# Performance work log

Measured on AMD Instinct MI355X. Metric: run time of the kernel, lower is better.

The kernel has to match this reference:

```python
import jax, jax.numpy as jnp
import numpy as np

B, S, D, KC = 32, 4096, 64, 256  # batch*heads, seq_len, head_dim, compressed dim


def setup_inputs() -> dict:
    key = jax.random.key(0)
    ks = jax.random.split(key, 7)
    return {
        "Q": jax.random.normal(ks[0], (B, S, D), dtype=jnp.float32),
        "K": jax.random.normal(ks[1], (B, S, D), dtype=jnp.float32),
        "V": jax.random.normal(ks[2], (B, S, D), dtype=jnp.float32),
        "E_w": jax.random.normal(ks[3], (KC, S), dtype=jnp.float32) * (1.0 / np.sqrt(S)),
        "E_b": jax.random.normal(ks[4], (KC,), dtype=jnp.float32) * 0.01,
        "F_w": jax.random.normal(ks[5], (KC, S), dtype=jnp.float32) * (1.0 / np.sqrt(S)),
        "F_b": jax.random.normal(ks[6], (KC,), dtype=jnp.float32) * 0.01,
    }


def reference(Q, K, V, E_w, E_b, F_w, F_b):
    # K: [B,S,D] -> transpose -> [B,D,S]; E proj over seq axis -> [B,D,KC]
    Ke = jnp.einsum("bsd,ks->bdk", K, E_w) + E_b  # [B, D, KC]
    # scores: Q @ E(K) -> [B, S, KC], scaled by sqrt(head_dim)
    scale = jnp.sqrt(jnp.asarray(D, dtype=Q.dtype))
    P = jnp.einsum("bsd,bdk->bsk", Q, Ke) / scale
    # causal mask: torch.triu(ones(S, KC)) keeps (i, j) where j >= i
    i = jnp.arange(S)[:, None]
    j = jnp.arange(KC)[None, :]
    keep = j >= i  # [S, KC]
    P = jnp.where(keep[None, :, :], P, jnp.asarray(-1e10, dtype=P.dtype))
    P = jax.nn.softmax(P, axis=-1)  # dropout p=0.0 -> identity
    # V: [B,S,D] -> [B,D,S]; F proj -> [B,D,KC]; transpose -> [B,KC,D]
    Vf = jnp.einsum("bsd,ks->bkd", V, F_w) + F_b[None, :, None]  # [B, KC, D]
    out = jnp.einsum("bsk,bkd->bsd", P, Vf)  # [B, S, D]
    return out
```

## Files before the change

kernel.cpp:

```cpp
#include <hip/hip_runtime.h>
#include <hip/hip_bf16.h>
#include <math.h>

#define NB  32
#define NS  4096
#define ND  64
#define NKC 256
#define ASTR 72
#define PSTR 260
#define PBSTR 264

typedef __attribute__((ext_vector_type(8))) short short8;
typedef __attribute__((ext_vector_type(4))) short sv4;
typedef __attribute__((ext_vector_type(4))) float f32x4;

__device__ __forceinline__ short f2bf(float f) {
    union { float f; unsigned u; } v; v.f = f;
    return (short)((v.u + 0x7FFFu + ((v.u >> 16) & 1u)) >> 16);
}
__device__ __forceinline__ float bf2f(short s) {
    union { unsigned u; float f; } v;
    v.u = ((unsigned)(unsigned short)s) << 16; return v.f;
}

__global__ __launch_bounds__(256) void proj_gemm(
    const float* __restrict__ Ew, const float* __restrict__ Fw,
    const float* __restrict__ K,  const float* __restrict__ V,
    float* __restrict__ KeT, float* __restrict__ Vf)
{
    const int b     = blockIdx.x;
    const int chunk = blockIdx.y;
    const int z     = blockIdx.z;
    const int mt = z >> 1, mm = z & 1;
    const float* __restrict__ A  = mm ? Fw : Ew;
    const float* __restrict__ Bg = mm ? V  : K;
    float* __restrict__ Cout     = mm ? Vf : KeT;

    const int t = threadIdx.x, wave = t >> 6, lane = t & 63;
    const int lm = lane & 15, g = lane >> 4;
    __shared__ short As[64 * ASTR];
    __shared__ short Bs[64 * ASTR];
    const int k0 = mt * 64;
    const size_t bBase = (size_t)b * NS * ND;

    f32x4 acc[4];
#pragma unroll
    for (int i = 0; i < 4; ++i) acc[i] = (f32x4){0.f, 0.f, 0.f, 0.f};

    for (int s0 = chunk * 1024; s0 < chunk * 1024 + 1024; s0 += 64) {
#pragma unroll
        for (int i = 0; i < 4; ++i) {
            int row = i * 16 + (t >> 4), q = t & 15;
            float4 v = *(const float4*)&A[(size_t)(k0 + row) * NS + s0 + q * 4];
            sv4 sv; sv.x = f2bf(v.x); sv.y = f2bf(v.y); sv.z = f2bf(v.z); sv.w = f2bf(v.w);
            *(sv4*)&As[row * ASTR + q * 4] = sv;
        }
        {
            int dB = t & 31, sB = t >> 5;
            float2 v[8];
#pragma unroll
            for (int i = 0; i < 8; ++i)
                v[i] = *(const float2*)&Bg[bBase + (size_t)(s0 + sB * 8 + i) * ND + dB * 2];
            short8 w0, w1;
#pragma unroll
            for (int i = 0; i < 8; ++i) { w0[i] = f2bf(v[i].x); w1[i] = f2bf(v[i].y); }
            *(short8*)&Bs[(dB * 2 + 0) * ASTR + sB * 8] = w0;
            *(short8*)&Bs[(dB * 2 + 1) * ASTR + sB * 8] = w1;
        }
        __syncthreads();
#pragma unroll
        for (int ks = 0; ks < 64; ks += 32) {
            short8 a = *(const short8*)&As[(wave * 16 + lm) * ASTR + ks + g * 8];
#pragma unroll
            for (int nt = 0; nt < 4; ++nt) {
                short8 bb = *(const short8*)&Bs[(nt * 16 + lm) * ASTR + ks + g * 8];
                acc[nt] = __builtin_amdgcn_mfma_f32_16x16x32_bf16(a, bb, acc[nt], 0, 0, 0);
            }
        }
        __syncthreads();
    }
#pragma unroll
    for (int r = 0; r < 4; ++r) {
        int kc = k0 + wave * 16 + g * 4 + r;
#pragma unroll
        for (int nt = 0; nt < 4; ++nt)
            atomicAdd(&Cout[((size_t)b * NKC + kc) * ND + nt * 16 + lm], acc[nt][r]);
    }
}

__global__ __launch_bounds__(256) void convert_bias(
    const float* __restrict__ KeT, const float* __restrict__ Vf,
    const float* __restrict__ Eb,  const float* __restrict__ Fb,
    short* __restrict__ KeTb, short* __restrict__ VfTb)
{
    const int b = blockIdx.y, t = threadIdx.x;
    const int k = blockIdx.x * 32 + (t >> 3), dq = t & 7;
    const size_t off = ((size_t)b * NKC + k) * ND + dq * 8;

    float4 a0 = *(const float4*)&KeT[off], a1 = *(const float4*)&KeT[off + 4];
    float eb = Eb[k];
    short8 w;
    w[0] = f2bf(a0.x + eb); w[1] = f2bf(a0.y + eb); w[2] = f2bf(a0.z + eb); w[3] = f2bf(a0.w + eb);
    w[4] = f2bf(a1.x + eb); w[5] = f2bf(a1.y + eb); w[6] = f2bf(a1.z + eb); w[7] = f2bf(a1.w + eb);
    *(short8*)&KeTb[off] = w;

    float4 v0 = *(const float4*)&Vf[off], v1 = *(const float4*)&Vf[off + 4];
    float fb = Fb[k];
    float vv[8] = {v0.x, v0.y, v0.z, v0.w, v1.x, v1.y, v1.z, v1.w};
#pragma unroll
    for (int j = 0; j < 8; ++j)
        VfTb[((size_t)b * ND + dq * 8 + j) * NKC + k] = f2bf(vv[j] + fb);
}

__global__ __launch_bounds__(256) void attn_fused(
    const float* __restrict__ Q, const short* __restrict__ KeTb,
    const short* __restrict__ VfTb, float* __restrict__ out)
{
    const int x = blockIdx.x, b = blockIdx.y, t = threadIdx.x;

    if (x >= 8) {
        const int ch = x - 8;
        __shared__ float part[4][65];
        __shared__ float mv[64];
        const int d = t >> 2, seg = t & 3;
        const short* vp = &VfTb[((size_t)b * ND + d) * NKC + seg * 64];
        float s = 0.f;
#pragma unroll
        for (int i = 0; i < 8; ++i) {
            short8 h = *(const short8*)&vp[i * 8];
#pragma unroll
            for (int j = 0; j < 8; ++j) s += bf2f(h[j]);
        }
        part[seg][d] = s;
        __syncthreads();
        if (t < 64)
            mv[t] = (part[0][t] + part[1][t] + part[2][t] + part[3][t]) * (1.f / 256.f);
        __syncthreads();
#pragma unroll
        for (int i = 0; i < 15; ++i) {
            int idx = i * 256 + t, row = idx >> 4, q = idx & 15;
            *(float4*)&out[((size_t)b * NS + 256 + ch * 240 + row) * ND + q * 4] =
                *(const float4*)&mv[q * 4];
        }
        return;
    }

    const int s0 = x * 32;
    const int wave = t >> 6, lane = t & 63, lm = lane & 15, g = lane >> 4;
    __shared__ short Qs[32 * ASTR];
    __shared__ float Ps[32 * PSTR];
    __shared__ short PsB[32 * PBSTR];

    {
        int row = t >> 3, dq = t & 7;
        size_t off = ((size_t)b * NS + s0 + row) * ND + dq * 8;
        float4 q0 = *(const float4*)&Q[off], q1 = *(const float4*)&Q[off + 4];
        short8 w;
        w[0] = f2bf(q0.x); w[1] = f2bf(q0.y); w[2] = f2bf(q0.z); w[3] = f2bf(q0.w);
        w[4] = f2bf(q1.x); w[5] = f2bf(q1.y); w[6] = f2bf(q1.z); w[7] = f2bf(q1.w);
        *(short8*)&Qs[row * ASTR + dq * 8] = w;
    }
    __syncthreads();

    const int rt = wave & 1, kh = wave >> 1;
#pragma unroll
    for (int kk = 0; kk < 8; ++kk) {
        int kt = kh * 8 + kk;
        f32x4 acc = (f32x4){0.f, 0.f, 0.f, 0.f};
#pragma unroll
        for (int ks = 0; ks < 64; ks += 32) {
            short8 a  = *(const short8*)&Qs[(rt * 16 + lm) * ASTR + ks + g * 8];
            short8 bb = *(const short8*)&KeTb[((size_t)b * NKC + kt * 16 + lm) * ND + ks + g * 8];
            acc = __builtin_amdgcn_mfma_f32_16x16x32_bf16(a, bb, acc, 0, 0, 0);
        }
        int col = kt * 16 + lm;
#pragma unroll
        for (int r = 0; r < 4; ++r) {
            int rowg = s0 + rt * 16 + g * 4 + r;
            Ps[(rt * 16 + g * 4 + r) * PSTR + col] =
                (col >= rowg) ? acc[r] * 0.125f : -1e30f;
        }
    }
    __syncthreads();

    for (int rr = wave * 8; rr < wave * 8 + 8; ++rr) {
        float v0 = Ps[rr * PSTR + lane],       v1 = Ps[rr * PSTR + lane + 64];
        float v2 = Ps[rr * PSTR + lane + 128], v3 = Ps[rr * PSTR + lane + 192];
        float m = fmaxf(fmaxf(v0, v1), fmaxf(v2, v3));
        for (int off = 32; off; off >>= 1) m = fmaxf(m, __shfl_xor(m, off, 64));
        float e0 = __expf(v0 - m), e1 = __expf(v1 - m);
        float e2 = __expf(v2 - m), e3 = __expf(v3 - m);
        float s = e0 + e1 + e2 + e3;
        for (int off = 32; off; off >>= 1) s += __shfl_xor(s, off, 64);
        float inv = 1.f / s;
        PsB[rr * PBSTR + lane]       = f2bf(e0 * inv);
        PsB[rr * PBSTR + lane + 64]  = f2bf(e1 * inv);
        PsB[rr * PBSTR + lane + 128] = f2bf(e2 * inv);
        PsB[rr * PBSTR + lane + 192] = f2bf(e3 * inv);
    }
    __syncthreads();

    const int dt = wave;
    f32x4 oa[2];
    oa[0] = (f32x4){0.f, 0.f, 0.f, 0.f};
    oa[1] = (f32x4){0.f, 0.f, 0.f, 0.f};
    for (int ks = x; ks < 8; ++ks) {
        short8 bb = *(const short8*)&VfTb[((size_t)b * ND + dt * 16 + lm) * NKC + ks * 32 + g * 8];
#pragma unroll
        for (int r2 = 0; r2 < 2; ++r2) {
            short8 a = *(const short8*)&PsB[(r2 * 16 + lm) * PBSTR + ks * 32 + g * 8];
            oa[r2] = __builtin_amdgcn_mfma_f32_16x16x32_bf16(a, bb, oa[r2], 0, 0, 0);
        }
    }
#pragma unroll
    for (int r2 = 0; r2 < 2; ++r2)
#pragma unroll
        for (int r = 0; r < 4; ++r)
            out[((size_t)b * NS + s0 + r2 * 16 + g * 4 + r) * ND + dt * 16 + lm] = oa[r2][r];
}

extern "C" void kernel_launch(void* const* d_in, const int* in_sizes, int n_in,
                              void* d_out, int out_size, void* d_ws, size_t ws_size,
                              hipStream_t stream) {
    (void)in_sizes; (void)n_in; (void)out_size; (void)ws_size;
    const float* Q  = (const float*)d_in[0];
    const float* K  = (const float*)d_in[1];
    const float* V  = (const float*)d_in[2];
    const float* Ew = (const float*)d_in[3];
    const float* Eb = (const float*)d_in[4];
    const float* Fw = (const float*)d_in[5];
    const float* Fb = (const float*)d_in[6];
    float* out = (float*)d_out;

    const size_t nKe = (size_t)NB * NKC * ND;
    float* KeT  = (float*)d_ws;
    float* Vf   = KeT + nKe;
    short* KeTb = (short*)(Vf + nKe);
    short* VfTb = KeTb + nKe;

    hipMemsetAsync(d_ws, 0, 2 * nKe * sizeof(float), stream);
    proj_gemm<<<dim3(NB, 4, 8), 256, 0, stream>>>(Ew, Fw, K, V, KeT, Vf);
    convert_bias<<<dim3(8, NB), 256, 0, stream>>>(KeT, Vf, Eb, Fb, KeTb, VfTb);
    attn_fused<<<dim3(24, NB), 256, 0, stream>>>(Q, KeTb, VfTb, out);
}
```

Before: 198.7 us.

## Prefetch next tile in projection GEMM, split seq chunks, transpose via LDS

```diff
diff --git a/kernel.cpp b/kernel.cpp
--- a/kernel.cpp
+++ b/kernel.cpp
@@ -42,32 +42,47 @@
     __shared__ short Bs[64 * ASTR];
     const int k0 = mt * 64;
     const size_t bBase = (size_t)b * NS * ND;
+    const int rowA = t >> 4, qA = t & 15;
+    const int dB = t & 31, sB = t >> 5;
 
     f32x4 acc[4];
 #pragma unroll
     for (int i = 0; i < 4; ++i) acc[i] = (f32x4){0.f, 0.f, 0.f, 0.f};
 
-    for (int s0 = chunk * 1024; s0 < chunk * 1024 + 1024; s0 += 64) {
+    const int sBeg = chunk * 512, sEnd = sBeg + 512;
+    float4 pa[4];
+    float2 pb[8];
+#pragma unroll
+    for (int i = 0; i < 4; ++i)
+        pa[i] = *(const float4*)&A[(size_t)(k0 + i * 16 + rowA) * NS + sBeg + qA * 4];
+#pragma unroll
+    for (int i = 0; i < 8; ++i)
+        pb[i] = *(const float2*)&Bg[bBase + (size_t)(sBeg + sB * 8 + i) * ND + dB * 2];
+
+    for (int s0 = sBeg; s0 < sEnd; s0 += 64) {
 #pragma unroll
         for (int i = 0; i < 4; ++i) {
-            int row = i * 16 + (t >> 4), q = t & 15;
-            float4 v = *(const float4*)&A[(size_t)(k0 + row) * NS + s0 + q * 4];
-            sv4 sv; sv.x = f2bf(v.x); sv.y = f2bf(v.y); sv.z = f2bf(v.z); sv.w = f2bf(v.w);
-            *(sv4*)&As[row * ASTR + q * 4] = sv;
+            sv4 sv;
+            sv.x = f2bf(pa[i].x); sv.y = f2bf(pa[i].y);
+            sv.z = f2bf(pa[i].z); sv.w = f2bf(pa[i].w);
+            *(sv4*)&As[(i * 16 + rowA) * ASTR + qA * 4] = sv;
         }
         {
-            int dB = t & 31, sB = t >> 5;
-            float2 v[8];
-#pragma unroll
-            for (int i = 0; i < 8; ++i)
-                v[i] = *(const float2*)&Bg[bBase + (size_t)(s0 + sB * 8 + i) * ND + dB * 2];
             short8 w0, w1;
 #pragma unroll
-            for (int i = 0; i < 8; ++i) { w0[i] = f2bf(v[i].x); w1[i] = f2bf(v[i].y); }
+            for (int i = 0; i < 8; ++i) { w0[i] = f2bf(pb[i].x); w1[i] = f2bf(pb[i].y); }
             *(short8*)&Bs[(dB * 2 + 0) * ASTR + sB * 8] = w0;
             *(short8*)&Bs[(dB * 2 + 1) * ASTR + sB * 8] = w1;
         }
         __syncthreads();
+        if (s0 + 64 < sEnd) {
+#pragma unroll
+            for (int i = 0; i < 4; ++i)
+                pa[i] = *(const float4*)&A[(size_t)(k0 + i * 16 + rowA) * NS + s0 + 64 + qA * 4];
+#pragma unroll
+            for (int i = 0; i < 8; ++i)
+                pb[i] = *(const float2*)&Bg[bBase + (size_t)(s0 + 64 + sB * 8 + i) * ND + dB * 2];
+        }
 #pragma unroll
         for (int ks = 0; ks < 64; ks += 32) {
             short8 a = *(const short8*)&As[(wave * 16 + lm) * ASTR + ks + g * 8];
@@ -93,23 +108,33 @@
     const float* __restrict__ Eb,  const float* __restrict__ Fb,
     short* __restrict__ KeTb, short* __restrict__ VfTb)
 {
-    const int b = blockIdx.y, t = threadIdx.x;
-    const int k = blockIdx.x * 32 + (t >> 3), dq = t & 7;
-    const size_t off = ((size_t)b * NKC + k) * ND + dq * 8;
-
-    float4 a0 = *(const float4*)&KeT[off], a1 = *(const float4*)&KeT[off + 4];
+    const int b = blockIdx.y, kt = blockIdx.x, t = threadIdx.x;
+    const int kk = t >> 4, dq = t & 15;
+    const int k = kt * 16 + kk;
+    __shared__ short Ls[16][68];
+
+    const size_t off = ((size_t)b * NKC + k) * ND + dq * 4;
+
+    float4 a = *(const float4*)&KeT[off];
     float eb = Eb[k];
-    short8 w;
-    w[0] = f2bf(a0.x + eb); w[1] = f2bf(a0.y + eb); w[2] = f2bf(a0.z + eb); w[3] = f2bf(a0.w + eb);
-    w[4] = f2bf(a1.x + eb); w[5] = f2bf(a1.y + eb); w[6] = f2bf(a1.z + eb); w[7] = f2bf(a1.w + eb);
-    *(short8*)&KeTb[off] = w;
-
-    float4 v0 = *(const float4*)&Vf[off], v1 = *(const float4*)&Vf[off + 4];
+    sv4 w;
+    w.x = f2bf(a.x + eb); w.y = f2bf(a.y + eb);
+    w.z = f2bf(a.z + eb); w.w = f2bf(a.w + eb);
+    *(sv4*)&KeTb[off] = w;
+
+    float4 v = *(const float4*)&Vf[off];
     float fb = Fb[k];
-    float vv[8] = {v0.x, v0.y, v0.z, v0.w, v1.x, v1.y, v1.z, v1.w};
-#pragma unroll
-    for (int j = 0; j < 8; ++j)
-        VfTb[((size_t)b * ND + dq * 8 + j) * NKC + k] = f2bf(vv[j] + fb);
+    sv4 u;
+    u.x = f2bf(v.x + fb); u.y = f2bf(v.y + fb);
+    u.z = f2bf(v.z + fb); u.w = f2bf(v.w + fb);
+    *(sv4*)&Ls[kk][dq * 4] = u;
+    __syncthreads();
+
+    const int d = t >> 2, ks = t & 3;
+    sv4 o;
+    o.x = Ls[ks * 4 + 0][d]; o.y = Ls[ks * 4 + 1][d];
+    o.z = Ls[ks * 4 + 2][d]; o.w = Ls[ks * 4 + 3][d];
+    *(sv4*)&VfTb[((size_t)b * ND + d) * NKC + kt * 16 + ks * 4] = o;
 }
 
 __global__ __launch_bounds__(256) void attn_fused(
@@ -239,7 +264,7 @@
     short* VfTb = KeTb + nKe;
 
     hipMemsetAsync(d_ws, 0, 2 * nKe * sizeof(float), stream);
-    proj_gemm<<<dim3(NB, 4, 8), 256, 0, stream>>>(Ew, Fw, K, V, KeT, Vf);
-    convert_bias<<<dim3(8, NB), 256, 0, stream>>>(KeT, Vf, Eb, Fb, KeTb, VfTb);
+    proj_gemm<<<dim3(NB, 8, 8), 256, 0, stream>>>(Ew, Fw, K, V, KeT, Vf);
+    convert_bias<<<dim3(16, NB), 256, 0, stream>>>(KeT, Vf, Eb, Fb, KeTb, VfTb);
     attn_fused<<<dim3(24, NB), 256, 0, stream>>>(Q, KeTb, VfTb, out);
 }
```

Measured after the change: 191.1 us. 1.04x faster.
